# Kernel optimization log

Measured on AMD Instinct MI355X. Metric: run time of the kernel, lower is better.

Reference implementation:

```python
import jax, jax.numpy as jnp
import numpy as np

B, T, V, D, OUT = 32, 100, 10000, 128, 1000
CODE_P = 0.003  # ~30 active codes per visit


def gru_dir(x3, whh, bhh, reverse):
    """x3: [B,T,3F] precomputed input-side gates (W_ih x + b_ih). PyTorch GRU math."""
    F = whh.shape[1]
    h0 = jnp.zeros((x3.shape[0], F), x3.dtype)

    def step(h, xt):
        gh = h @ whh.T + bhh
        xr, xz, xn = jnp.split(xt, 3, -1)
        hr, hz, hn = jnp.split(gh, 3, -1)
        r = jax.nn.sigmoid(xr + hr)
        z = jax.nn.sigmoid(xz + hz)
        n = jnp.tanh(xn + r * hn)
        h_new = (1.0 - z) * n + z * h
        return h_new, h_new

    _, hs = jax.lax.scan(step, h0, jnp.swapaxes(x3, 0, 1), reverse=reverse)
    return jnp.swapaxes(hs, 0, 1)  # [B,T,F]


def setup_inputs() -> dict:
    key = jax.random.key(0)
    ks = jax.random.split(key, 16)
    s = lambda k, *sh: jax.random.normal(k, sh, dtype=jnp.float32) * 0.05
    # multi-hot visits, ~0/1 with density CODE_P; force code 0 present so no all-zero visit
    x = (jax.random.uniform(ks[0], (B, T, V)) < CODE_P).astype(jnp.float32)
    x = x.at[:, :, 0].set(1.0)
    return {
        "batchdata": x,
        "emb": s(ks[1], V, D),
        "wih_f": s(ks[2], 3 * D, D), "whh_f": s(ks[3], 3 * D, D),
        "bih_f": jnp.zeros((3 * D,), jnp.float32), "bhh_f": jnp.zeros((3 * D,), jnp.float32),
        "wih_b": s(ks[4], 3 * D, D), "whh_b": s(ks[5], 3 * D, D),
        "bih_b": jnp.zeros((3 * D,), jnp.float32), "bhh_b": jnp.zeros((3 * D,), jnp.float32),
        "attn_w": s(ks[6], 2 * D, 1), "attn_b": jnp.zeros((1,), jnp.float32),
        "comb_w": s(ks[7], D, 4 * D), "comb_b": jnp.zeros((D,), jnp.float32),
        "fc_w": s(ks[8], OUT, D), "fc_b": jnp.zeros((OUT,), jnp.float32),
    }


def reference(batchdata, emb, wih_f, whh_f, bih_f, bhh_f, wih_b, whh_b, bih_b, bhh_b,
              attn_w, attn_b, comb_w, comb_b, fc_w, fc_b):
    # multihot_to_embedding: sum of embedding rows where visit==1 == multihot @ table
    e = jnp.einsum('btv,vd->btd', batchdata, emb)          # [B,T,D]
    mask = jnp.any(e != 0, axis=2)                          # [B,T]
    # DipoleLayer: bidirectional GRU (hidden=D each dir), dropout in eval mode = identity
    xf = jnp.einsum('btf,gf->btg', e, wih_f) + bih_f
    xb = jnp.einsum('btf,gf->btg', e, wih_b) + bih_b
    hf = gru_dir(xf, whh_f, bhh_f, reverse=False)
    hb = gru_dir(xb, whh_b, bhh_b, reverse=True)
    h = jnp.concatenate([hf, hb], axis=-1)                  # [B,T,2D]
    # location-based attention over timesteps
    scores = (h @ attn_w)[..., 0] + attn_b[0]               # [B,T]
    scores = jnp.where(mask, scores, jnp.float32(-1e9))
    a = jax.nn.softmax(scores, axis=-1)
    c = jnp.einsum('bt,btf->bf', a, h)                      # [B,2D] context
    last = jnp.sum(mask.astype(jnp.int32), axis=-1) - 1     # last valid visit
    h_last = h[jnp.arange(h.shape[0]), last]                # [B,2D]
    feat = jnp.tanh(jnp.concatenate([c, h_last], -1) @ comb_w.T + comb_b)  # [B,D]
    logits = feat @ fc_w.T + fc_b                           # [B,OUT]
    return logits
```

## Files before the change

### kernel.cpp

```cpp
#include <hip/hip_runtime.h>
#include <math.h>

#define BB 32
#define TT 100
#define VV 10000
#define DD 128
#define OUTN 1000
#define G3 384

__global__ __launch_bounds__(256) void k_embed(
    const float* __restrict__ x, const float* __restrict__ emb,
    float* __restrict__ e, int* __restrict__ mask)
{
    const int bt  = blockIdx.x;
    const int tid = threadIdx.x;
    __shared__ int   s_cnt;
    __shared__ int   s_any;
    __shared__ int   s_idx[256];
    __shared__ float s_val[256];
    if (tid == 0) { s_cnt = 0; s_any = 0; }
    __syncthreads();

    const float4* x4 = (const float4*)(x + (size_t)bt * VV);
    for (int i = tid; i < VV / 4; i += 256) {
        float4 v = x4[i];
        if (v.x != 0.f) { int p = atomicAdd(&s_cnt, 1); if (p < 256) { s_idx[p] = 4*i+0; s_val[p] = v.x; } }
        if (v.y != 0.f) { int p = atomicAdd(&s_cnt, 1); if (p < 256) { s_idx[p] = 4*i+1; s_val[p] = v.y; } }
        if (v.z != 0.f) { int p = atomicAdd(&s_cnt, 1); if (p < 256) { s_idx[p] = 4*i+2; s_val[p] = v.z; } }
        if (v.w != 0.f) { int p = atomicAdd(&s_cnt, 1); if (p < 256) { s_idx[p] = 4*i+3; s_val[p] = v.w; } }
    }
    __syncthreads();
    int cnt = s_cnt; if (cnt > 256) cnt = 256;
    if (tid < DD) {
        float a0 = 0.f, a1 = 0.f, a2 = 0.f, a3 = 0.f;
        int i = 0;
        for (; i + 3 < cnt; i += 4) {
            a0 += s_val[i+0] * emb[(size_t)s_idx[i+0] * DD + tid];
            a1 += s_val[i+1] * emb[(size_t)s_idx[i+1] * DD + tid];
            a2 += s_val[i+2] * emb[(size_t)s_idx[i+2] * DD + tid];
            a3 += s_val[i+3] * emb[(size_t)s_idx[i+3] * DD + tid];
        }
        for (; i < cnt; ++i)
            a0 += s_val[i] * emb[(size_t)s_idx[i] * DD + tid];
        float acc = (a0 + a1) + (a2 + a3);
        e[(size_t)bt * DD + tid] = acc;
        if (acc != 0.f) s_any = 1;
    }
    __syncthreads();
    if (tid == 0) mask[bt] = s_any;
}

__global__ __launch_bounds__(256) void k_gates(
    const float* __restrict__ e,
    const float* __restrict__ wih_f, const float* __restrict__ bih_f,
    const float* __restrict__ wih_b, const float* __restrict__ bih_b,
    float* __restrict__ x3)
{
    const int r0  = blockIdx.x * 8;
    const int tid = threadIdx.x;
    __shared__ __align__(16) float se[8][DD];
    for (int i = tid; i < 8 * DD; i += 256)
        se[i >> 7][i & 127] = e[(size_t)(r0 + (i >> 7)) * DD + (i & 127)];
    __syncthreads();

    for (int cc = 0; cc < 3; ++cc) {
        const int col = tid + cc * 256;
        const float* wrow;
        float bias;
        if (col < G3) { wrow = wih_f + (size_t)col * DD;        bias = bih_f[col]; }
        else          { wrow = wih_b + (size_t)(col - G3) * DD; bias = bih_b[col - G3]; }
        float acc[8];
        #pragma unroll
        for (int r = 0; r < 8; ++r) acc[r] = 0.f;
        const float4* w4 = (const float4*)wrow;
        for (int k4 = 0; k4 < DD / 4; ++k4) {
            float4 w = w4[k4];
            #pragma unroll
            for (int r = 0; r < 8; ++r) {
                float4 ev = *(const float4*)&se[r][4 * k4];
                acc[r] += ev.x * w.x + ev.y * w.y + ev.z * w.z + ev.w * w.w;
            }
        }
        #pragma unroll
        for (int r = 0; r < 8; ++r)
            x3[(size_t)(r0 + r) * 768 + col] = acc[r] + bias;
    }
}

__device__ __forceinline__ float4 ld_pin_b128(const float4* p)
{
    float4 r;
    asm volatile("global_load_dwordx4 %0, %1, off" : "=v"(r) : "v"(p));
    return r;
}

__global__ __launch_bounds__(512, 1) void k_gru(
    const float* __restrict__ x3,
    const float* __restrict__ whh_f, const float* __restrict__ bhh_f,
    const float* __restrict__ whh_b, const float* __restrict__ bhh_b,
    float* __restrict__ h_all)
{
    const int dir = blockIdx.x & 1;
    const int b   = blockIdx.x >> 1;
    const int tid = threadIdx.x;
    const int g   = tid & 127;
    const int kq  = tid >> 7;
    const int kb  = kq * 32;
    const float* whh = dir ? whh_b : whh_f;
    const float* bhh = dir ? bhh_b : bhh_f;

    const float4* pr4 = (const float4*)(whh + (size_t)(g         ) * DD + kb);
    const float4* pz4 = (const float4*)(whh + (size_t)(DD     + g) * DD + kb);
    const float4* pn4 = (const float4*)(whh + (size_t)(2 * DD + g) * DD + kb);

#define Q8(M) M(0) M(1) M(2) M(3) M(4) M(5) M(6) M(7)
#define DECLW(i) float4 wr##i = ld_pin_b128(pr4 + (i)); \
                 float4 wz##i = ld_pin_b128(pz4 + (i)); \
                 float4 wn##i = ld_pin_b128(pn4 + (i));
    Q8(DECLW)
#undef DECLW
    asm volatile("s_waitcnt vmcnt(0)" ::: "memory");
    __builtin_amdgcn_sched_barrier(0);

    float bhr = 0.f, bhz = 0.f, bhn = 0.f;
    if (tid < DD) { bhr = bhh[g]; bhz = bhh[DD + g]; bhn = bhh[2 * DD + g]; }

    __shared__ __align__(16) float h_lds[DD];
    __shared__ float p_lds[9 * DD];
    float h_reg = 0.f;
    if (tid < DD) h_lds[tid] = 0.f;

    float xr = 0.f, xz = 0.f, xn = 0.f;
    {
        const float* x3p = x3 + (size_t)(b * TT + (dir ? TT - 1 : 0)) * 768 + dir * G3;
        if (tid < DD) { xr = x3p[g]; xz = x3p[DD + g]; xn = x3p[2 * DD + g]; }
    }
    __syncthreads();

    for (int t = 0; t < TT; ++t) {
        const int te = dir ? (TT - 1 - t) : t;

        float nxr = 0.f, nxz = 0.f, nxn = 0.f;
        if (t + 1 < TT) {
            const int tn = dir ? (TT - 2 - t) : (t + 1);
            const float* x3n = x3 + (size_t)(b * TT + tn) * 768 + dir * G3;
            if (tid < DD) { nxr = x3n[g]; nxz = x3n[DD + g]; nxn = x3n[2 * DD + g]; }
        }

        float ar0 = 0.f, ar1 = 0.f, az0 = 0.f, az1 = 0.f, an0 = 0.f, an1 = 0.f;
#define FMA(i) { float4 hv = *(const float4*)&h_lds[kb + 4 * (i)]; \
        (((i)&1) ? ar1 : ar0) += wr##i.x*hv.x + wr##i.y*hv.y + wr##i.z*hv.z + wr##i.w*hv.w; \
        (((i)&1) ? az1 : az0) += wz##i.x*hv.x + wz##i.y*hv.y + wz##i.z*hv.z + wz##i.w*hv.w; \
        (((i)&1) ? an1 : an0) += wn##i.x*hv.x + wn##i.y*hv.y + wn##i.z*hv.z + wn##i.w*hv.w; }
        Q8(FMA)
#undef FMA
        const float pr = ar0 + ar1, pz = az0 + az1, pn = an0 + an1;

        if (kq) {
            const int q = (kq - 1) * 3;
            p_lds[(q + 0) * DD + g] = pr;
            p_lds[(q + 1) * DD + g] = pz;
            p_lds[(q + 2) * DD + g] = pn;
        }
        __syncthreads();

        if (tid < DD) {
            float hr = pr + p_lds[0*DD+g] + p_lds[3*DD+g] + p_lds[6*DD+g] + bhr;
            float hz = pz + p_lds[1*DD+g] + p_lds[4*DD+g] + p_lds[7*DD+g] + bhz;
            float hn = pn + p_lds[2*DD+g] + p_lds[5*DD+g] + p_lds[8*DD+g] + bhn;
            float r  = __builtin_amdgcn_rcpf(1.f + __expf(-(xr + hr)));
            float z  = __builtin_amdgcn_rcpf(1.f + __expf(-(xz + hz)));
            float e2 = __expf(2.f * (xn + r * hn));
            float n  = 1.f - 2.f * __builtin_amdgcn_rcpf(e2 + 1.f);
            float hnew = n + z * (h_reg - n);
            h_reg = hnew;
            h_lds[g] = hnew;
            h_all[(size_t)((dir * BB + b) * TT + te) * DD + g] = hnew;
        }
        __syncthreads();
        xr = nxr; xz = nxz; xn = nxn;
    }
#undef Q8
}

__global__ __launch_bounds__(256) void k_attn_logits(
    const float* __restrict__ h_all, const int* __restrict__ mask,
    const float* __restrict__ attn_w, const float* __restrict__ attn_b,
    const float* __restrict__ comb_w, const float* __restrict__ comb_b,
    const float* __restrict__ fc_w, const float* __restrict__ fc_b,
    float* __restrict__ out)
{
    const int b   = blockIdx.x;
    const int tid = threadIdx.x;
    __shared__ float s_aw[256];
    __shared__ float s_sc[128];
    __shared__ int   s_m[128];
    __shared__ float s_red[128];
    __shared__ __align__(16) float s_ch[512];
    __shared__ __align__(16) float s_feat[128];

    s_aw[tid] = attn_w[tid];
    int m = 0;
    if (tid < 128) {
        m = (tid < TT) ? mask[b * TT + tid] : 0;
        s_m[tid] = m;
    }
    __syncthreads();
    for (int s = 64; s > 0; s >>= 1) {
        if (tid < s) s_m[tid] += s_m[tid + s];
        __syncthreads();
    }
    const int last = s_m[0] - 1;

    const float* hf = h_all + (size_t)(0 * BB + b) * TT * DD;
    const float* hb = h_all + (size_t)(1 * BB + b) * TT * DD;

    float sc = -1e9f;
    if (tid < TT) {
        float a = attn_b[0];
        const float4* hf4 = (const float4*)(hf + (size_t)tid * DD);
        const float4* hb4 = (const float4*)(hb + (size_t)tid * DD);
        for (int k = 0; k < DD / 4; ++k) {
            float4 v = hf4[k];
            a += v.x * s_aw[4*k] + v.y * s_aw[4*k+1] + v.z * s_aw[4*k+2] + v.w * s_aw[4*k+3];
        }
        for (int k = 0; k < DD / 4; ++k) {
            float4 v = hb4[k];
            a += v.x * s_aw[DD+4*k] + v.y * s_aw[DD+4*k+1] + v.z * s_aw[DD+4*k+2] + v.w * s_aw[DD+4*k+3];
        }
        sc = m ? a : -1e9f;
    }
    if (tid < 128) { s_sc[tid] = sc; s_red[tid] = sc; }
    __syncthreads();
    for (int s = 64; s > 0; s >>= 1) {
        if (tid < s) s_red[tid] = fmaxf(s_red[tid], s_red[tid + s]);
        __syncthreads();
    }
    const float mx = s_red[0];
    __syncthreads();
    float ex = 0.f;
    if (tid < 128) { ex = __expf(s_sc[tid] - mx); s_sc[tid] = ex; s_red[tid] = ex; }
    __syncthreads();
    for (int s = 64; s > 0; s >>= 1) {
        if (tid < s) s_red[tid] += s_red[tid + s];
        __syncthreads();
    }
    const float inv = 1.f / s_red[0];
    __syncthreads();

    {
        const int fl = tid & 127;
        const float* hp = (tid < 128) ? hf : hb;
        float csum = 0.f;
        for (int t = 0; t < TT; ++t)
            csum += s_sc[t] * hp[(size_t)t * DD + fl];
        s_ch[tid]       = csum * inv;
        s_ch[256 + tid] = hp[(size_t)last * DD + fl];
    }
    __syncthreads();

    if (tid < 128) {
        float a = comb_b[tid];
        const float4* cw = (const float4*)(comb_w + (size_t)tid * 512);
        for (int k = 0; k < 128; ++k) {
            float4 w4 = cw[k];
            float4 v4 = *(const float4*)&s_ch[4 * k];
            a += w4.x * v4.x + w4.y * v4.y + w4.z * v4.z + w4.w * v4.w;
        }
        s_feat[tid] = tanhf(a);
    }
    __syncthreads();

    #pragma unroll
    for (int j = 0; j < 4; ++j) {
        const int o = j * 256 + tid;
        if (o < OUTN) {
            float a = fc_b[o];
            const float4* w4 = (const float4*)(fc_w + (size_t)o * DD);
            for (int k = 0; k < DD / 4; ++k) {
                float4 w = w4[k];
                float4 v = *(const float4*)&s_feat[4 * k];
                a += w.x * v.x + w.y * v.y + w.z * v.z + w.w * v.w;
            }
            out[(size_t)b * OUTN + o] = a;
        }
    }
}

extern "C" void kernel_launch(void* const* d_in, const int* in_sizes, int n_in,
                              void* d_out, int out_size, void* d_ws, size_t ws_size,
                              hipStream_t stream)
{
    const float* x      = (const float*)d_in[0];
    const float* emb    = (const float*)d_in[1];
    const float* wih_f  = (const float*)d_in[2];
    const float* whh_f  = (const float*)d_in[3];
    const float* bih_f  = (const float*)d_in[4];
    const float* bhh_f  = (const float*)d_in[5];
    const float* wih_b  = (const float*)d_in[6];
    const float* whh_b  = (const float*)d_in[7];
    const float* bih_b  = (const float*)d_in[8];
    const float* bhh_b  = (const float*)d_in[9];
    const float* attn_w = (const float*)d_in[10];
    const float* attn_b = (const float*)d_in[11];
    const float* comb_w = (const float*)d_in[12];
    const float* comb_b = (const float*)d_in[13];
    const float* fc_w   = (const float*)d_in[14];
    const float* fc_b   = (const float*)d_in[15];
    float* out = (float*)d_out;

    float* ws    = (float*)d_ws;
    float* e     = ws;
    float* x3    = ws + 409600;
    float* h_all = ws + 2867200;
    int*   mask  = (int*)(ws + 3686400);

    k_embed       <<<BB * TT,     256, 0, stream>>>(x, emb, e, mask);
    k_gates       <<<(BB * TT)/8, 256, 0, stream>>>(e, wih_f, bih_f, wih_b, bih_b, x3);
    k_gru         <<<2 * BB,      512, 0, stream>>>(x3, whh_f, bhh_f, whh_b, bhh_b, h_all);
    k_attn_logits <<<BB,          256, 0, stream>>>(h_all, mask, attn_w, attn_b, comb_w, comb_b, fc_w, fc_b, out);
}
```

Measured before the change: 362.1 us.

## Process two batch rows per GRU block and reload weights from cache each step

Each GRU block now advances two sequences (b0, b1) for one direction, sharing every recurrent weight load across both hidden states, so the grid halves from 64 to 32 blocks. The weights are no longer pinned in registers once before the loop. They are reloaded each timestep through an opaque pointer, which relies on L1/L2 hits to cut register pressure. This adds per-step global load latency to the serial recurrence and leaves fewer blocks to spread across the GPU, in exchange for doing twice the FMA work per synchronisation.

Measured after the change: 914.2 us. +152.5%, slower.

```diff
diff --git a/kernel.cpp b/kernel.cpp
--- a/kernel.cpp
+++ b/kernel.cpp
@@ -87,13 +87,6 @@
     }
 }
 
-__device__ __forceinline__ float4 ld_pin_b128(const float4* p)
-{
-    float4 r;
-    asm volatile("global_load_dwordx4 %0, %1, off" : "=v"(r) : "v"(p));
-    return r;
-}
-
 __global__ __launch_bounds__(512, 1) void k_gru(
     const float* __restrict__ x3,
     const float* __restrict__ whh_f, const float* __restrict__ bhh_f,
@@ -101,7 +94,8 @@
     float* __restrict__ h_all)
 {
     const int dir = blockIdx.x & 1;
-    const int b   = blockIdx.x >> 1;
+    const int bp  = blockIdx.x >> 1;
+    const int b0  = bp * 2, b1 = b0 + 1;
     const int tid = threadIdx.x;
     const int g   = tid & 127;
     const int kq  = tid >> 7;
@@ -113,72 +107,102 @@
     const float4* pz4 = (const float4*)(whh + (size_t)(DD     + g) * DD + kb);
     const float4* pn4 = (const float4*)(whh + (size_t)(2 * DD + g) * DD + kb);
 
-#define Q8(M) M(0) M(1) M(2) M(3) M(4) M(5) M(6) M(7)
-#define DECLW(i) float4 wr##i = ld_pin_b128(pr4 + (i)); \
-                 float4 wz##i = ld_pin_b128(pz4 + (i)); \
-                 float4 wn##i = ld_pin_b128(pn4 + (i));
-    Q8(DECLW)
-#undef DECLW
-    asm volatile("s_waitcnt vmcnt(0)" ::: "memory");
-    __builtin_amdgcn_sched_barrier(0);
-
     float bhr = 0.f, bhz = 0.f, bhn = 0.f;
     if (tid < DD) { bhr = bhh[g]; bhz = bhh[DD + g]; bhn = bhh[2 * DD + g]; }
 
-    __shared__ __align__(16) float h_lds[DD];
-    __shared__ float p_lds[9 * DD];
-    float h_reg = 0.f;
-    if (tid < DD) h_lds[tid] = 0.f;
-
-    float xr = 0.f, xz = 0.f, xn = 0.f;
+    __shared__ __align__(16) float h_lds[2][DD];
+    __shared__ float p_lds[2][9 * DD];
+    float h0 = 0.f, h1 = 0.f;
+    if (tid < 2 * DD) h_lds[tid >> 7][tid & 127] = 0.f;
+
+    float x0r = 0.f, x0z = 0.f, x0n = 0.f, x1r = 0.f, x1z = 0.f, x1n = 0.f;
     {
-        const float* x3p = x3 + (size_t)(b * TT + (dir ? TT - 1 : 0)) * 768 + dir * G3;
-        if (tid < DD) { xr = x3p[g]; xz = x3p[DD + g]; xn = x3p[2 * DD + g]; }
-    }
-    __syncthreads();
-
+        const int te0 = dir ? TT - 1 : 0;
+        const float* p0 = x3 + (size_t)(b0 * TT + te0) * 768 + dir * G3;
+        const float* p1 = x3 + (size_t)(b1 * TT + te0) * 768 + dir * G3;
+        if (tid < DD) {
+            x0r = p0[g]; x0z = p0[DD + g]; x0n = p0[2 * DD + g];
+            x1r = p1[g]; x1z = p1[DD + g]; x1n = p1[2 * DD + g];
+        }
+    }
+    __syncthreads();
+
+#define Q8(M) M(0) M(1) M(2) M(3) M(4) M(5) M(6) M(7)
     for (int t = 0; t < TT; ++t) {
         const int te = dir ? (TT - 1 - t) : t;
 
-        float nxr = 0.f, nxz = 0.f, nxn = 0.f;
-        if (t + 1 < TT) {
+        const float4* pr = pr4; asm volatile("" : "+v"(pr));
+        const float4* pz = pz4; asm volatile("" : "+v"(pz));
+        const float4* pn = pn4; asm volatile("" : "+v"(pn));
+
+#define DECLW(i) const float4 wr##i = pr[i]; const float4 wz##i = pz[i]; const float4 wn##i = pn[i];
+        Q8(DECLW)
+#undef DECLW
+
+        float n0r = 0.f, n0z = 0.f, n0n = 0.f, n1r = 0.f, n1z = 0.f, n1n = 0.f;
+        if (t + 1 < TT && tid < DD) {
             const int tn = dir ? (TT - 2 - t) : (t + 1);
-            const float* x3n = x3 + (size_t)(b * TT + tn) * 768 + dir * G3;
-            if (tid < DD) { nxr = x3n[g]; nxz = x3n[DD + g]; nxn = x3n[2 * DD + g]; }
-        }
-
-        float ar0 = 0.f, ar1 = 0.f, az0 = 0.f, az1 = 0.f, an0 = 0.f, an1 = 0.f;
-#define FMA(i) { float4 hv = *(const float4*)&h_lds[kb + 4 * (i)]; \
-        (((i)&1) ? ar1 : ar0) += wr##i.x*hv.x + wr##i.y*hv.y + wr##i.z*hv.z + wr##i.w*hv.w; \
-        (((i)&1) ? az1 : az0) += wz##i.x*hv.x + wz##i.y*hv.y + wz##i.z*hv.z + wz##i.w*hv.w; \
-        (((i)&1) ? an1 : an0) += wn##i.x*hv.x + wn##i.y*hv.y + wn##i.z*hv.z + wn##i.w*hv.w; }
-        Q8(FMA)
-#undef FMA
-        const float pr = ar0 + ar1, pz = az0 + az1, pn = an0 + an1;
+            const float* q0 = x3 + (size_t)(b0 * TT + tn) * 768 + dir * G3;
+            const float* q1 = x3 + (size_t)(b1 * TT + tn) * 768 + dir * G3;
+            n0r = q0[g]; n0z = q0[DD + g]; n0n = q0[2 * DD + g];
+            n1r = q1[g]; n1z = q1[DD + g]; n1n = q1[2 * DD + g];
+        }
+
+        float ar0 = 0.f, az0 = 0.f, an0 = 0.f, ar1 = 0.f, az1 = 0.f, an1 = 0.f;
+#define FMAB(i) { \
+        const float4 u0 = *(const float4*)&h_lds[0][kb + 4 * (i)]; \
+        const float4 u1 = *(const float4*)&h_lds[1][kb + 4 * (i)]; \
+        ar0 += wr##i.x*u0.x + wr##i.y*u0.y + wr##i.z*u0.z + wr##i.w*u0.w; \
+        az0 += wz##i.x*u0.x + wz##i.y*u0.y + wz##i.z*u0.z + wz##i.w*u0.w; \
+        an0 += wn##i.x*u0.x + wn##i.y*u0.y + wn##i.z*u0.z + wn##i.w*u0.w; \
+        ar1 += wr##i.x*u1.x + wr##i.y*u1.y + wr##i.z*u1.z + wr##i.w*u1.w; \
+        az1 += wz##i.x*u1.x + wz##i.y*u1.y + wz##i.z*u1.z + wz##i.w*u1.w; \
+        an1 += wn##i.x*u1.x + wn##i.y*u1.y + wn##i.z*u1.z + wn##i.w*u1.w; }
+        Q8(FMAB)
+#undef FMAB
 
         if (kq) {
             const int q = (kq - 1) * 3;
-            p_lds[(q + 0) * DD + g] = pr;
-            p_lds[(q + 1) * DD + g] = pz;
-            p_lds[(q + 2) * DD + g] = pn;
+            p_lds[0][(q + 0) * DD + g] = ar0;
+            p_lds[0][(q + 1) * DD + g] = az0;
+            p_lds[0][(q + 2) * DD + g] = an0;
+            p_lds[1][(q + 0) * DD + g] = ar1;
+            p_lds[1][(q + 1) * DD + g] = az1;
+            p_lds[1][(q + 2) * DD + g] = an1;
         }
         __syncthreads();
 
         if (tid < DD) {
-            float hr = pr + p_lds[0*DD+g] + p_lds[3*DD+g] + p_lds[6*DD+g] + bhr;
-            float hz = pz + p_lds[1*DD+g] + p_lds[4*DD+g] + p_lds[7*DD+g] + bhz;
-            float hn = pn + p_lds[2*DD+g] + p_lds[5*DD+g] + p_lds[8*DD+g] + bhn;
-            float r  = __builtin_amdgcn_rcpf(1.f + __expf(-(xr + hr)));
-            float z  = __builtin_amdgcn_rcpf(1.f + __expf(-(xz + hz)));
-            float e2 = __expf(2.f * (xn + r * hn));
-            float n  = 1.f - 2.f * __builtin_amdgcn_rcpf(e2 + 1.f);
-            float hnew = n + z * (h_reg - n);
-            h_reg = hnew;
-            h_lds[g] = hnew;
-            h_all[(size_t)((dir * BB + b) * TT + te) * DD + g] = hnew;
-        }
-        __syncthreads();
-        xr = nxr; xz = nxz; xn = nxn;
+            {
+                float hr = ar0 + p_lds[0][0*DD+g] + p_lds[0][3*DD+g] + p_lds[0][6*DD+g] + bhr;
+                float hz = az0 + p_lds[0][1*DD+g] + p_lds[0][4*DD+g] + p_lds[0][7*DD+g] + bhz;
+                float hn = an0 + p_lds[0][2*DD+g] + p_lds[0][5*DD+g] + p_lds[0][8*DD+g] + bhn;
+                float r  = __builtin_amdgcn_rcpf(1.f + __expf(-(x0r + hr)));
+                float z  = __builtin_amdgcn_rcpf(1.f + __expf(-(x0z + hz)));
+                float e2 = __expf(2.f * (x0n + r * hn));
+                float n  = 1.f - 2.f * __builtin_amdgcn_rcpf(e2 + 1.f);
+                float hnew = n + z * (h0 - n);
+                h0 = hnew;
+                h_lds[0][g] = hnew;
+                h_all[(size_t)((dir * BB + b0) * TT + te) * DD + g] = hnew;
+            }
+            {
+                float hr = ar1 + p_lds[1][0*DD+g] + p_lds[1][3*DD+g] + p_lds[1][6*DD+g] + bhr;
+                float hz = az1 + p_lds[1][1*DD+g] + p_lds[1][4*DD+g] + p_lds[1][7*DD+g] + bhz;
+                float hn = an1 + p_lds[1][2*DD+g] + p_lds[1][5*DD+g] + p_lds[1][8*DD+g] + bhn;
+                float r  = __builtin_amdgcn_rcpf(1.f + __expf(-(x1r + hr)));
+                float z  = __builtin_amdgcn_rcpf(1.f + __expf(-(x1z + hz)));
+                float e2 = __expf(2.f * (x1n + r * hn));
+                float n  = 1.f - 2.f * __builtin_amdgcn_rcpf(e2 + 1.f);
+                float hnew = n + z * (h1 - n);
+                h1 = hnew;
+                h_lds[1][g] = hnew;
+                h_all[(size_t)((dir * BB + b1) * TT + te) * DD + g] = hnew;
+            }
+        }
+        __syncthreads();
+        x0r = n0r; x0z = n0z; x0n = n0n;
+        x1r = n1r; x1z = n1z; x1n = n1n;
     }
 #undef Q8
 }
@@ -317,6 +341,6 @@
 
     k_embed       <<<BB * TT,     256, 0, stream>>>(x, emb, e, mask);
     k_gates       <<<(BB * TT)/8, 256, 0, stream>>>(e, wih_f, bih_f, wih_b, bih_b, x3);
-    k_gru         <<<2 * BB,      512, 0, stream>>>(x3, whh_f, bhh_f, whh_b, bhh_b, h_all);
+    k_gru         <<<BB,          512, 0, stream>>>(x3, whh_f, bhh_f, whh_b, bhh_b, h_all);
     k_attn_logits <<<BB,          256, 0, stream>>>(h_all, mask, attn_w, attn_b, comb_w, comb_b, fc_w, fc_b, out);
 }
```
